# Optimization experiments

Hardware: AMD Instinct MI355X
Metric: run time of the kernel (lower is better)

## Reference

```python
import jax, jax.numpy as jnp
import numpy as np

N, E, D, L = 100000, 640000, 128, 5
BN_EPS = 1e-5


def setup_inputs() -> dict:
    key = jax.random.key(0)
    ks = jax.random.split(key, 10)
    x = jax.random.normal(ks[0], (N, D), jnp.float32)
    edge_index = jax.random.randint(ks[1], (2, E), 0, N, dtype=jnp.int32)
    W1 = jax.random.normal(ks[2], (L, D, 2 * D), jnp.float32) / np.float32(np.sqrt(D))
    b1 = jnp.zeros((L, 2 * D), jnp.float32)
    bn1_g = jnp.ones((L, 2 * D), jnp.float32)
    bn1_b = jnp.zeros((L, 2 * D), jnp.float32)
    bn1_m = 0.1 * jax.random.normal(ks[3], (L, 2 * D), jnp.float32)
    bn1_v = jax.random.uniform(ks[4], (L, 2 * D), jnp.float32) + 0.5
    W2 = jax.random.normal(ks[5], (L, 2 * D, D), jnp.float32) / np.float32(np.sqrt(2 * D))
    b2 = jnp.zeros((L, D), jnp.float32)
    bno_g = jnp.ones((L, D), jnp.float32)
    bno_b = jnp.zeros((L, D), jnp.float32)
    bno_m = 0.1 * jax.random.normal(ks[6], (L, D), jnp.float32)
    bno_v = jax.random.uniform(ks[7], (L, D), jnp.float32) + 0.5
    return {"x": x, "edge_index": edge_index, "W1": W1, "b1": b1,
            "bn1_g": bn1_g, "bn1_b": bn1_b, "bn1_m": bn1_m, "bn1_v": bn1_v,
            "W2": W2, "b2": b2,
            "bno_g": bno_g, "bno_b": bno_b, "bno_m": bno_m, "bno_v": bno_v}


def _bn(z, g, b, m, v):
    # BatchNorm1d in eval mode: running stats
    return (z - m) * jax.lax.rsqrt(v + BN_EPS) * g + b


def reference(x, edge_index, W1, b1, bn1_g, bn1_b, bn1_m, bn1_v,
              W2, b2, bno_g, bno_b, bno_m, bno_v):
    src, dst = edge_index[0], edge_index[1]
    h = x
    for l in range(L):
        # GINConv with eps=0: (1+eps)*h_i + sum_{j->i} h_j
        agg = h + jax.ops.segment_sum(h[src], dst, num_segments=N)  # [N, d]
        z = jax.nn.relu(_bn(agg @ W1[l] + b1[l], bn1_g[l], bn1_b[l], bn1_m[l], bn1_v[l]))
        h = _bn(z @ W2[l] + b2[l], bno_g[l], bno_b[l], bno_m[l], bno_v[l])
        if l != L - 1:
            h = jax.nn.relu(h)
        # dropout is identity in eval mode
    return h
```

## Files before the change

kernel.cpp:

```cpp
#include <hip/hip_runtime.h>

#define ND 100000
#define DD 128
#define HH 256
#define EE 640000
#define LL 5

#define GS 152
#define ZS 280

typedef __attribute__((ext_vector_type(8))) short short8;
typedef __attribute__((ext_vector_type(4))) short short4v;
typedef __attribute__((ext_vector_type(4))) float f32x4;
typedef __attribute__((ext_vector_type(8))) _Float16 half8;
typedef __attribute__((ext_vector_type(4))) _Float16 half4;
typedef __attribute__((ext_vector_type(2))) _Float16 half2v;

static __device__ __forceinline__ short f2h(float f) {
    return __builtin_bit_cast(short, (_Float16)f);
}

static __device__ __forceinline__ half2v pk2(float a, float b) {
    return __builtin_bit_cast(half2v, __builtin_amdgcn_cvt_pkrtz(a, b));
}

__global__ __launch_bounds__(256) void setup(
    const float* __restrict__ W1, const float* __restrict__ b1,
    const float* __restrict__ g1, const float* __restrict__ bb1,
    const float* __restrict__ m1, const float* __restrict__ v1,
    const float* __restrict__ W2, const float* __restrict__ b2,
    const float* __restrict__ g2, const float* __restrict__ bb2,
    const float* __restrict__ m2, const float* __restrict__ v2,
    const float* __restrict__ x, const int* __restrict__ dst,
    short* __restrict__ W1p, float* __restrict__ b1e,
    short* __restrict__ W2p, float* __restrict__ b2e,
    short* __restrict__ hb, int* __restrict__ cnt)
{
    int bx = blockIdx.x;
    int tid = threadIdx.x;
    if (bx < 640) {
        int id = bx * 256 + tid;
        if (id < LL * HH * DD) {
            int l = id >> 15;
            int rem = id & 32767;
            {
                int n = rem >> 7, k = rem & 127;
                float s = g1[l * HH + n] * rsqrtf(v1[l * HH + n] + 1e-5f);
                W1p[id] = f2h(W1[l * 32768 + k * HH + n] * s);
            }
            {
                int n2 = rem >> 8, k2 = rem & 255;
                float s = g2[l * DD + n2] * rsqrtf(v2[l * DD + n2] + 1e-5f);
                W2p[id] = f2h(W2[l * 32768 + k2 * DD + n2] * s);
            }
        }
        if (id < LL * HH) {
            float s = g1[id] * rsqrtf(v1[id] + 1e-5f);
            b1e[id] = (b1[id] - m1[id]) * s + bb1[id];
        }
        if (id < LL * DD) {
            float s = g2[id] * rsqrtf(v2[id] + 1e-5f);
            b2e[id] = (b2[id] - m2[id]) * s + bb2[id];
        }
    } else if (bx < 13140) {
        int i = (bx - 640) * 256 + tid;
        float4 v = reinterpret_cast<const float4*>(x)[i];
        half2v p0 = pk2(v.x, v.y);
        half2v p1 = pk2(v.z, v.w);
        half4 hv = __builtin_shufflevector(p0, p1, 0, 1, 2, 3);
        reinterpret_cast<short4v*>(hb)[i] = __builtin_bit_cast(short4v, hv);
    } else {
        int e = (bx - 13140) * 256 + tid;
        if (e < EE) atomicAdd(&cnt[dst[e]], 1);
    }
}

__global__ __launch_bounds__(256) void scan_block(int* __restrict__ cnt, int* __restrict__ bsum)
{
    __shared__ int buf[256];
    int tid = threadIdx.x;
    int idx = blockIdx.x * 256 + tid;
    int v = (idx < ND) ? cnt[idx] : 0;
    buf[tid] = v;
    __syncthreads();
    int sum = v;
    for (int off = 1; off < 256; off <<= 1) {
        int t = (tid >= off) ? buf[tid - off] : 0;
        __syncthreads();
        sum += t;
        buf[tid] = sum;
        __syncthreads();
    }
    if (idx < ND) cnt[idx] = sum;
    if (tid == 255) bsum[blockIdx.x] = sum;
}

__global__ __launch_bounds__(256) void apply_offs2(const int* __restrict__ cnt,
                                                   const int* __restrict__ bsum,
                                                   int* __restrict__ rowst)
{
    __shared__ int sred[256];
    int tid = threadIdx.x;
    int partial = 0;
    for (int i = tid; i < blockIdx.x; i += 256) partial += bsum[i];
    sred[tid] = partial;
    __syncthreads();
    for (int off = 128; off > 0; off >>= 1) {
        if (tid < off) sred[tid] += sred[tid + off];
        __syncthreads();
    }
    int boff = sred[0];
    int idx = blockIdx.x * 256 + tid;
    if (idx < ND) rowst[idx + 1] = cnt[idx] + boff;
    if (idx == 0) rowst[0] = 0;
}

__global__ __launch_bounds__(256) void fill_csr(const int* __restrict__ src,
                                                const int* __restrict__ dst,
                                                const int* __restrict__ rowstart,
                                                int* __restrict__ cursor,
                                                int* __restrict__ csr)
{
    int e = blockIdx.x * 256 + threadIdx.x;
    if (e < EE) {
        int d = dst[e];
        int p = atomicAdd(&cursor[d], 1);
        csr[rowstart[d] + p] = src[e];
    }
}

__global__ __launch_bounds__(256) void gather_agg(
    const short* __restrict__ hb_in,
    const int* __restrict__ rowst,
    const int* __restrict__ csr,
    short* __restrict__ aggb)
{
    const int row = blockIdx.x * 16 + (threadIdx.x >> 4);
    const int ch = (threadIdx.x & 15) * 8;
    if (row >= ND) return;

    half8 acc = __builtin_bit_cast(half8,
        *reinterpret_cast<const short8*>(&hb_in[(size_t)row * DD + ch]));
    int i = rowst[row];
    int deg = rowst[row + 1] - i;
    while (deg > 0) {
        int c = deg < 8 ? deg : 8;
        half8 a[8];
        #pragma unroll
        for (int k = 0; k < 8; ++k)
            if (k < c)
                a[k] = __builtin_bit_cast(half8,
                    *reinterpret_cast<const short8*>(&hb_in[(size_t)csr[i + k] * DD + ch]));
        #pragma unroll
        for (int k = 0; k < 8; ++k)
            if (k < c) acc = acc + a[k];
        i += c; deg -= c;
    }
    *reinterpret_cast<short8*>(&aggb[(size_t)row * DD + ch]) =
        __builtin_bit_cast(short8, acc);
}

__global__ __launch_bounds__(1024, 8) void mlp(
    const short* __restrict__ aggb,
    const short* __restrict__ W1l,
    const float* __restrict__ b1l,
    const short* __restrict__ W2l,
    const float* __restrict__ b2l,
    short* __restrict__ hb_out, float* __restrict__ f_out, int last)
{
    __shared__ __attribute__((aligned(16))) short sU[64 * ZS];

    const int tid = threadIdx.x;
    const int r0 = blockIdx.x * 64;
    const int wave = tid >> 6;
    const int lane = tid & 63;
    const int quad = lane >> 4;
    const int l16 = lane & 15;

    {
        int row = tid >> 4;
        int ch = (tid & 15) * 8;
        int grow = r0 + row;
        short8 v = {};
        if (grow < ND)
            v = *reinterpret_cast<const short8*>(&aggb[(size_t)grow * DD + ch]);
        *reinterpret_cast<short8*>(&sU[row * GS + ch]) = v;
    }

    const int zrow = wave * 16 + l16;
    half8 aw1[4];
    for (int ks = 0; ks < 4; ++ks)
        aw1[ks] = __builtin_bit_cast(half8,
            *reinterpret_cast<const short8*>(&W1l[zrow * DD + ks * 32 + quad * 8]));
    float4 bias1 = *reinterpret_cast<const float4*>(&b1l[wave * 16 + quad * 4]);
    __syncthreads();

    const f32x4 zero4 = {0.f, 0.f, 0.f, 0.f};
    f32x4 acc1[4];
    for (int nt = 0; nt < 4; ++nt) acc1[nt] = zero4;

    for (int ks = 0; ks < 4; ++ks) {
        int kofs = ks * 32 + quad * 8;
        for (int nt = 0; nt < 4; ++nt) {
            half8 bn = __builtin_bit_cast(half8,
                *reinterpret_cast<const short8*>(&sU[(nt * 16 + l16) * GS + kofs]));
            acc1[nt] = __builtin_amdgcn_mfma_f32_16x16x32_f16(aw1[ks], bn, acc1[nt], 0, 0, 0);
        }
    }
    __syncthreads();

    {
        int zc = wave * 16 + quad * 4;
        for (int nt = 0; nt < 4; ++nt) {
            int node = nt * 16 + l16;
            half2v p0 = pk2(fmaxf(acc1[nt][0] + bias1.x, 0.f),
                            fmaxf(acc1[nt][1] + bias1.y, 0.f));
            half2v p1 = pk2(fmaxf(acc1[nt][2] + bias1.z, 0.f),
                            fmaxf(acc1[nt][3] + bias1.w, 0.f));
            half4 hv = __builtin_shufflevector(p0, p1, 0, 1, 2, 3);
            *reinterpret_cast<short4v*>(&sU[node * ZS + zc]) = __builtin_bit_cast(short4v, hv);
        }
    }

    const int ct16 = wave >> 1;
    const int nh = wave & 1;
    const int orow = ct16 * 16 + l16;
    half8 w_cur = __builtin_bit_cast(half8,
        *reinterpret_cast<const short8*>(&W2l[orow * HH + quad * 8]));
    float4 bias2 = *reinterpret_cast<const float4*>(&b2l[ct16 * 16 + quad * 4]);
    __syncthreads();

    f32x4 acc2[2];
    for (int nt = 0; nt < 2; ++nt) acc2[nt] = zero4;

    for (int ks = 0; ks < 8; ++ks) {
        half8 w_next;
        if (ks < 7)
            w_next = __builtin_bit_cast(half8,
                *reinterpret_cast<const short8*>(&W2l[orow * HH + (ks + 1) * 32 + quad * 8]));
        int kofs = ks * 32 + quad * 8;
        for (int nt = 0; nt < 2; ++nt) {
            int node = nh * 32 + nt * 16 + l16;
            half8 bn = __builtin_bit_cast(half8,
                *reinterpret_cast<const short8*>(&sU[node * ZS + kofs]));
            acc2[nt] = __builtin_amdgcn_mfma_f32_16x16x32_f16(w_cur, bn, acc2[nt], 0, 0, 0);
        }
        w_cur = w_next;
    }

    {
        int oc = ct16 * 16 + quad * 4;
        for (int nt = 0; nt < 2; ++nt) {
            int node = r0 + nh * 32 + nt * 16 + l16;
            if (node < ND) {
                float v0 = acc2[nt][0] + bias2.x;
                float v1 = acc2[nt][1] + bias2.y;
                float v2 = acc2[nt][2] + bias2.z;
                float v3 = acc2[nt][3] + bias2.w;
                if (!last) {
                    half2v p0 = pk2(fmaxf(v0, 0.f), fmaxf(v1, 0.f));
                    half2v p1 = pk2(fmaxf(v2, 0.f), fmaxf(v3, 0.f));
                    half4 hv = __builtin_shufflevector(p0, p1, 0, 1, 2, 3);
                    *reinterpret_cast<short4v*>(&hb_out[(size_t)node * DD + oc]) =
                        __builtin_bit_cast(short4v, hv);
                } else {
                    float4 st; st.x = v0; st.y = v1; st.z = v2; st.w = v3;
                    *reinterpret_cast<float4*>(&f_out[(size_t)node * DD + oc]) = st;
                }
            }
        }
    }
}

extern "C" void kernel_launch(void* const* d_in, const int* in_sizes, int n_in,
                              void* d_out, int out_size, void* d_ws, size_t ws_size,
                              hipStream_t stream)
{
    const float* x  = (const float*)d_in[0];
    const int* ei   = (const int*)d_in[1];
    const int* src  = ei;
    const int* dst  = ei + EE;
    const float* W1 = (const float*)d_in[2];
    const float* b1 = (const float*)d_in[3];
    const float* g1 = (const float*)d_in[4];
    const float* bb1= (const float*)d_in[5];
    const float* m1 = (const float*)d_in[6];
    const float* v1 = (const float*)d_in[7];
    const float* W2 = (const float*)d_in[8];
    const float* b2 = (const float*)d_in[9];
    const float* g2 = (const float*)d_in[10];
    const float* bb2= (const float*)d_in[11];
    const float* m2 = (const float*)d_in[12];
    const float* v2 = (const float*)d_in[13];

    char* w = (char*)d_ws;
    short* hbuf  = (short*)w;
    short* aggb  = (short*)(w + 25600000);
    short* W1p   = (short*)(w + 51200000);
    short* W2p   = (short*)(w + 51527680);
    float* b1e   = (float*)(w + 51855360);
    float* b2e   = (float*)(w + 51860480);
    int*   cnt   = (int*)  (w + 51863040);
    int*   cursor= (int*)  (w + 52263040);
    int*   rowst = (int*)  (w + 52663040);
    int*   csr   = (int*)  (w + 53063072);
    int*   bsum  = (int*)  (w + 55623136);
    float* out   = (float*)d_out;

    (void)hipMemsetAsync(cnt, 0, 800000, stream);
    setup<<<15640, 256, 0, stream>>>(W1, b1, g1, bb1, m1, v1,
                                     W2, b2, g2, bb2, m2, v2,
                                     x, dst, W1p, b1e, W2p, b2e, hbuf, cnt);
    scan_block<<<391, 256, 0, stream>>>(cnt, bsum);
    apply_offs2<<<391, 256, 0, stream>>>(cnt, bsum, rowst);
    fill_csr<<<2500, 256, 0, stream>>>(src, dst, rowst, cursor, csr);

    for (int l = 0; l < LL; ++l) {
        gather_agg<<<6250, 256, 0, stream>>>(hbuf, rowst, csr, aggb);
        mlp<<<1563, 1024, 0, stream>>>(aggb,
                                       W1p + l * 32768, b1e + l * HH,
                                       W2p + l * 32768, b2e + l * DD,
                                       hbuf, out, (l == LL - 1) ? 1 : 0);
    }
}
```

Baseline: 582.8 us.

## Fuse neighbor aggregation and MLP into one per-layer kernel with ping-pong buffers

Merges the gather-aggregate kernel and the two-GEMM MLP kernel into one kernel that handles 16 nodes per 256-thread block. The aggregated features stay in shared memory instead of going through a global buffer, which removes a write and re-read of the aggregate array and one launch per layer. Node features now alternate between two buffers so a layer never overwrites its own input. In exchange, each small block reloads the W1 and W2 tiles from global memory or cache, so weight traffic rises and the MFMA work per block is smaller.

```diff
diff --git a/kernel.cpp b/kernel.cpp
--- a/kernel.cpp
+++ b/kernel.cpp
@@ -129,50 +129,22 @@
     }
 }
 
-__global__ __launch_bounds__(256) void gather_agg(
+__global__ __launch_bounds__(256, 8) void layer_fused(
     const short* __restrict__ hb_in,
     const int* __restrict__ rowst,
     const int* __restrict__ csr,
-    short* __restrict__ aggb)
-{
-    const int row = blockIdx.x * 16 + (threadIdx.x >> 4);
-    const int ch = (threadIdx.x & 15) * 8;
-    if (row >= ND) return;
-
-    half8 acc = __builtin_bit_cast(half8,
-        *reinterpret_cast<const short8*>(&hb_in[(size_t)row * DD + ch]));
-    int i = rowst[row];
-    int deg = rowst[row + 1] - i;
-    while (deg > 0) {
-        int c = deg < 8 ? deg : 8;
-        half8 a[8];
-        #pragma unroll
-        for (int k = 0; k < 8; ++k)
-            if (k < c)
-                a[k] = __builtin_bit_cast(half8,
-                    *reinterpret_cast<const short8*>(&hb_in[(size_t)csr[i + k] * DD + ch]));
-        #pragma unroll
-        for (int k = 0; k < 8; ++k)
-            if (k < c) acc = acc + a[k];
-        i += c; deg -= c;
-    }
-    *reinterpret_cast<short8*>(&aggb[(size_t)row * DD + ch]) =
-        __builtin_bit_cast(short8, acc);
-}
-
-__global__ __launch_bounds__(1024, 8) void mlp(
-    const short* __restrict__ aggb,
     const short* __restrict__ W1l,
     const float* __restrict__ b1l,
     const short* __restrict__ W2l,
     const float* __restrict__ b2l,
     short* __restrict__ hb_out, float* __restrict__ f_out, int last)
 {
-    __shared__ __attribute__((aligned(16))) short sU[64 * ZS];
+    __shared__ __attribute__((aligned(16))) short sG[16 * GS];
+    __shared__ __attribute__((aligned(16))) short sZ[16 * ZS];
 
     const int tid = threadIdx.x;
-    const int r0 = blockIdx.x * 64;
-    const int wave = tid >> 6;
+    const int r0 = blockIdx.x * 16;
+    const int w = tid >> 6;
     const int lane = tid & 63;
     const int quad = lane >> 4;
     const int l16 = lane & 15;
@@ -181,92 +153,97 @@
         int row = tid >> 4;
         int ch = (tid & 15) * 8;
         int grow = r0 + row;
-        short8 v = {};
-        if (grow < ND)
-            v = *reinterpret_cast<const short8*>(&aggb[(size_t)grow * DD + ch]);
-        *reinterpret_cast<short8*>(&sU[row * GS + ch]) = v;
-    }
-
-    const int zrow = wave * 16 + l16;
-    half8 aw1[4];
-    for (int ks = 0; ks < 4; ++ks)
-        aw1[ks] = __builtin_bit_cast(half8,
-            *reinterpret_cast<const short8*>(&W1l[zrow * DD + ks * 32 + quad * 8]));
-    float4 bias1 = *reinterpret_cast<const float4*>(&b1l[wave * 16 + quad * 4]);
+        half8 acc = __builtin_bit_cast(half8,
+            *reinterpret_cast<const short8*>(&hb_in[(size_t)grow * DD + ch]));
+        int i = rowst[grow];
+        int deg = rowst[grow + 1] - i;
+        while (deg > 0) {
+            int c = deg < 8 ? deg : 8;
+            half8 a[8];
+            #pragma unroll
+            for (int k = 0; k < 8; ++k)
+                if (k < c)
+                    a[k] = __builtin_bit_cast(half8,
+                        *reinterpret_cast<const short8*>(&hb_in[(size_t)csr[i + k] * DD + ch]));
+            #pragma unroll
+            for (int k = 0; k < 8; ++k)
+                if (k < c) acc = acc + a[k];
+            i += c; deg -= c;
+        }
+        *reinterpret_cast<short8*>(&sG[row * GS + ch]) = __builtin_bit_cast(short8, acc);
+    }
     __syncthreads();
 
     const f32x4 zero4 = {0.f, 0.f, 0.f, 0.f};
     f32x4 acc1[4];
-    for (int nt = 0; nt < 4; ++nt) acc1[nt] = zero4;
-
+    #pragma unroll
+    for (int ct = 0; ct < 4; ++ct) acc1[ct] = zero4;
+
+    #pragma unroll
     for (int ks = 0; ks < 4; ++ks) {
         int kofs = ks * 32 + quad * 8;
-        for (int nt = 0; nt < 4; ++nt) {
-            half8 bn = __builtin_bit_cast(half8,
-                *reinterpret_cast<const short8*>(&sU[(nt * 16 + l16) * GS + kofs]));
-            acc1[nt] = __builtin_amdgcn_mfma_f32_16x16x32_f16(aw1[ks], bn, acc1[nt], 0, 0, 0);
-        }
+        half8 bn = __builtin_bit_cast(half8,
+            *reinterpret_cast<const short8*>(&sG[l16 * GS + kofs]));
+        half8 aw[4];
+        #pragma unroll
+        for (int ct = 0; ct < 4; ++ct)
+            aw[ct] = __builtin_bit_cast(half8,
+                *reinterpret_cast<const short8*>(&W1l[(w * 64 + ct * 16 + l16) * DD + kofs]));
+        #pragma unroll
+        for (int ct = 0; ct < 4; ++ct)
+            acc1[ct] = __builtin_amdgcn_mfma_f32_16x16x32_f16(aw[ct], bn, acc1[ct], 0, 0, 0);
+    }
+
+    #pragma unroll
+    for (int ct = 0; ct < 4; ++ct) {
+        int zc = w * 64 + ct * 16 + quad * 4;
+        float4 bi = *reinterpret_cast<const float4*>(&b1l[zc]);
+        half2v p0 = pk2(fmaxf(acc1[ct][0] + bi.x, 0.f),
+                        fmaxf(acc1[ct][1] + bi.y, 0.f));
+        half2v p1 = pk2(fmaxf(acc1[ct][2] + bi.z, 0.f),
+                        fmaxf(acc1[ct][3] + bi.w, 0.f));
+        half4 hv = __builtin_shufflevector(p0, p1, 0, 1, 2, 3);
+        *reinterpret_cast<short4v*>(&sZ[l16 * ZS + zc]) = __builtin_bit_cast(short4v, hv);
     }
     __syncthreads();
 
+    f32x4 acc2[2];
+    acc2[0] = zero4; acc2[1] = zero4;
+
+    #pragma unroll
+    for (int ks = 0; ks < 8; ++ks) {
+        int kofs = ks * 32 + quad * 8;
+        half8 bn = __builtin_bit_cast(half8,
+            *reinterpret_cast<const short8*>(&sZ[l16 * ZS + kofs]));
+        half8 aw[2];
+        #pragma unroll
+        for (int ct = 0; ct < 2; ++ct)
+            aw[ct] = __builtin_bit_cast(half8,
+                *reinterpret_cast<const short8*>(&W2l[(w * 32 + ct * 16 + l16) * HH + kofs]));
+        #pragma unroll
+        for (int ct = 0; ct < 2; ++ct)
+            acc2[ct] = __builtin_amdgcn_mfma_f32_16x16x32_f16(aw[ct], bn, acc2[ct], 0, 0, 0);
+    }
+
     {
-        int zc = wave * 16 + quad * 4;
-        for (int nt = 0; nt < 4; ++nt) {
-            int node = nt * 16 + l16;
-            half2v p0 = pk2(fmaxf(acc1[nt][0] + bias1.x, 0.f),
-                            fmaxf(acc1[nt][1] + bias1.y, 0.f));
-            half2v p1 = pk2(fmaxf(acc1[nt][2] + bias1.z, 0.f),
-                            fmaxf(acc1[nt][3] + bias1.w, 0.f));
-            half4 hv = __builtin_shufflevector(p0, p1, 0, 1, 2, 3);
-            *reinterpret_cast<short4v*>(&sU[node * ZS + zc]) = __builtin_bit_cast(short4v, hv);
-        }
-    }
-
-    const int ct16 = wave >> 1;
-    const int nh = wave & 1;
-    const int orow = ct16 * 16 + l16;
-    half8 w_cur = __builtin_bit_cast(half8,
-        *reinterpret_cast<const short8*>(&W2l[orow * HH + quad * 8]));
-    float4 bias2 = *reinterpret_cast<const float4*>(&b2l[ct16 * 16 + quad * 4]);
-    __syncthreads();
-
-    f32x4 acc2[2];
-    for (int nt = 0; nt < 2; ++nt) acc2[nt] = zero4;
-
-    for (int ks = 0; ks < 8; ++ks) {
-        half8 w_next;
-        if (ks < 7)
-            w_next = __builtin_bit_cast(half8,
-                *reinterpret_cast<const short8*>(&W2l[orow * HH + (ks + 1) * 32 + quad * 8]));
-        int kofs = ks * 32 + quad * 8;
-        for (int nt = 0; nt < 2; ++nt) {
-            int node = nh * 32 + nt * 16 + l16;
-            half8 bn = __builtin_bit_cast(half8,
-                *reinterpret_cast<const short8*>(&sU[node * ZS + kofs]));
-            acc2[nt] = __builtin_amdgcn_mfma_f32_16x16x32_f16(w_cur, bn, acc2[nt], 0, 0, 0);
-        }
-        w_cur = w_next;
-    }
-
-    {
-        int oc = ct16 * 16 + quad * 4;
-        for (int nt = 0; nt < 2; ++nt) {
-            int node = r0 + nh * 32 + nt * 16 + l16;
-            if (node < ND) {
-                float v0 = acc2[nt][0] + bias2.x;
-                float v1 = acc2[nt][1] + bias2.y;
-                float v2 = acc2[nt][2] + bias2.z;
-                float v3 = acc2[nt][3] + bias2.w;
-                if (!last) {
-                    half2v p0 = pk2(fmaxf(v0, 0.f), fmaxf(v1, 0.f));
-                    half2v p1 = pk2(fmaxf(v2, 0.f), fmaxf(v3, 0.f));
-                    half4 hv = __builtin_shufflevector(p0, p1, 0, 1, 2, 3);
-                    *reinterpret_cast<short4v*>(&hb_out[(size_t)node * DD + oc]) =
-                        __builtin_bit_cast(short4v, hv);
-                } else {
-                    float4 st; st.x = v0; st.y = v1; st.z = v2; st.w = v3;
-                    *reinterpret_cast<float4*>(&f_out[(size_t)node * DD + oc]) = st;
-                }
+        int node = r0 + l16;
+        #pragma unroll
+        for (int ct = 0; ct < 2; ++ct) {
+            int oc = w * 32 + ct * 16 + quad * 4;
+            float4 bi = *reinterpret_cast<const float4*>(&b2l[oc]);
+            float v0 = acc2[ct][0] + bi.x;
+            float v1 = acc2[ct][1] + bi.y;
+            float v2 = acc2[ct][2] + bi.z;
+            float v3 = acc2[ct][3] + bi.w;
+            if (!last) {
+                half2v p0 = pk2(fmaxf(v0, 0.f), fmaxf(v1, 0.f));
+                half2v p1 = pk2(fmaxf(v2, 0.f), fmaxf(v3, 0.f));
+                half4 hv = __builtin_shufflevector(p0, p1, 0, 1, 2, 3);
+                *reinterpret_cast<short4v*>(&hb_out[(size_t)node * DD + oc]) =
+                    __builtin_bit_cast(short4v, hv);
+            } else {
+                float4 st; st.x = v0; st.y = v1; st.z = v2; st.w = v3;
+                *reinterpret_cast<float4*>(&f_out[(size_t)node * DD + oc]) = st;
             }
         }
     }
@@ -294,8 +271,8 @@
     const float* v2 = (const float*)d_in[13];
 
     char* w = (char*)d_ws;
-    short* hbuf  = (short*)w;
-    short* aggb  = (short*)(w + 25600000);
+    short* hbufA = (short*)w;
+    short* hbufB = (short*)(w + 25600000);
     short* W1p   = (short*)(w + 51200000);
     short* W2p   = (short*)(w + 51527680);
     float* b1e   = (float*)(w + 51855360);
@@ -310,16 +287,18 @@
     (void)hipMemsetAsync(cnt, 0, 800000, stream);
     setup<<<15640, 256, 0, stream>>>(W1, b1, g1, bb1, m1, v1,
                                      W2, b2, g2, bb2, m2, v2,
-                                     x, dst, W1p, b1e, W2p, b2e, hbuf, cnt);
+                                     x, dst, W1p, b1e, W2p, b2e, hbufA, cnt);
     scan_block<<<391, 256, 0, stream>>>(cnt, bsum);
     apply_offs2<<<391, 256, 0, stream>>>(cnt, bsum, rowst);
     fill_csr<<<2500, 256, 0, stream>>>(src, dst, rowst, cursor, csr);
 
+    short* hin = hbufA;
+    short* hout = hbufB;
     for (int l = 0; l < LL; ++l) {
-        gather_agg<<<6250, 256, 0, stream>>>(hbuf, rowst, csr, aggb);
-        mlp<<<1563, 1024, 0, stream>>>(aggb,
-                                       W1p + l * 32768, b1e + l * HH,
-                                       W2p + l * 32768, b2e + l * DD,
-                                       hbuf, out, (l == LL - 1) ? 1 : 0);
-    }
-}
+        layer_fused<<<6250, 256, 0, stream>>>(hin, rowst, csr,
+                                              W1p + l * 32768, b1e + l * HH,
+                                              W2p + l * 32768, b2e + l * DD,
+                                              hout, out, (l == LL - 1) ? 1 : 0);
+        short* t = hin; hin = hout; hout = t;
+    }
+}
```

Result: slower. 770.3 us (+32.2%).
